# Kernel tuning notes

Measured on AMD Instinct MI355X. Metric: run time of the kernel, lower is better.

Reference implementation:

```python
import jax, jax.numpy as jnp
import numpy as np

N_NODES = 50000
N_EDGES = 800000
HDIM = 128
N_RELS = 24


def setup_inputs() -> dict:
    key = jax.random.key(0)
    ks = jax.random.split(key, 7)
    h = jax.random.normal(ks[0], (N_NODES, HDIM), dtype=jnp.float32)
    # per-relation weights ('simple' regularizer: independent matrix per relation)
    W = jax.random.normal(ks[1], (N_RELS, HDIM, HDIM), dtype=jnp.float32) / np.sqrt(HDIM)
    W_loop = jax.random.normal(ks[2], (HDIM, HDIM), dtype=jnp.float32) / np.sqrt(HDIM)
    bias = jax.random.normal(ks[3], (HDIM,), dtype=jnp.float32) * 0.02
    src = jax.random.randint(ks[4], (N_EDGES,), 0, N_NODES, dtype=jnp.int32)
    dst = jax.random.randint(ks[5], (N_EDGES,), 0, N_NODES, dtype=jnp.int32)
    rel = jax.random.randint(ks[6], (N_EDGES,), 0, N_RELS, dtype=jnp.int32)
    return {"h": h, "W": W, "W_loop": W_loop, "bias": bias,
            "src": src, "dst": dst, "rel": rel}


def reference(h, W, W_loop, bias, src, dst, rel):
    """RGCN.forward(g, step=0): one RelGraphConv layer.

    msg_e  = h[src_e] @ W[rel_e]          (per-relation transform)
    agg_v  = mean_{e: dst_e = v} msg_e    (mean aggregation)
    out_v  = relu(agg_v + h_v @ W_loop + bias)   (self-loop + activation)
    skip=False, dropout=0 -> no skip-average, dropout is identity.
    """
    N, D = h.shape
    # Transform all node features by every relation matrix once: (R, N, D).
    # Then each edge gathers its (relation, source) row -- avoids gathering
    # a per-edge (E, D, D) weight tensor.
    Hr = jnp.einsum('nd,rde->rne', h, W)          # (R, N, D)
    msg = Hr[rel, src]                            # (E, D) gathered messages
    agg = jax.ops.segment_sum(msg, dst, num_segments=N)            # (N, D)
    deg = jax.ops.segment_sum(jnp.ones((msg.shape[0],), h.dtype), dst,
                              num_segments=N)                      # (N,)
    agg = agg / jnp.maximum(deg, 1.0)[:, None]    # mean aggregation
    out = jax.nn.relu(agg + h @ W_loop + bias)
    return out
```

## Files before the change

### kernel.cpp

```cpp
#include <hip/hip_runtime.h>
#include <hip/hip_bf16.h>

#define N_NODES 50000
#define N_EDGES 800000
#define HDIM    128
#define N_RELS  24

#define MAX_TILES  12524
#define SORTED_CAP (MAX_TILES * 64)
#define NSCAN_BLK  196
#define TPB        4

typedef __attribute__((ext_vector_type(8))) short bf16x8;
typedef __attribute__((ext_vector_type(4))) float f32x4;
typedef __attribute__((ext_vector_type(4))) unsigned int u32x4;

static __device__ __forceinline__ float bfbits2f(unsigned u) {
    return __uint_as_float(u << 16);
}
static __device__ __forceinline__ unsigned f2bfbits(float x) {
    union { __hip_bfloat16 b; unsigned short u; } cv;
    cv.b = __float2bfloat16(x);
    return (unsigned)cv.u;
}



__global__ void k_setup(const float* __restrict__ h,
                        const float* __restrict__ W,
                        const float* __restrict__ Wl,
                        const int* __restrict__ rel,
                        const int* __restrict__ dst,
                        unsigned short* __restrict__ hb,
                        unsigned short* __restrict__ Wbt,
                        unsigned short* __restrict__ Wlbt,
                        int* __restrict__ degi,
                        int* __restrict__ meta)
{
    __shared__ int lh[N_RELS];
    if (threadIdx.x < N_RELS) lh[threadIdx.x] = 0;
    __syncthreads();

    int stride = gridDim.x * blockDim.x;
    int tid = blockIdx.x * blockDim.x + threadIdx.x;

    const float4* h4 = (const float4*)h;
    for (int i = tid; i < N_NODES * HDIM / 4; i += stride) {
        float4 v = h4[i];
        uint2 o;
        o.x = f2bfbits(v.x) | (f2bfbits(v.y) << 16);
        o.y = f2bfbits(v.z) | (f2bfbits(v.w) << 16);
        ((uint2*)hb)[i] = o;
    }
    for (int i = tid; i < N_RELS * HDIM * HDIM / 4; i += stride) {
        int r = i >> 12, rem = i & 4095;
        int e = rem >> 5, kq = rem & 31;
        const float* wp = W + (r << 14) + (kq << 9) + e;
        uint2 o;
        o.x = f2bfbits(wp[0])   | (f2bfbits(wp[128]) << 16);
        o.y = f2bfbits(wp[256]) | (f2bfbits(wp[384]) << 16);
        ((uint2*)Wbt)[i] = o;
    }
    for (int i = tid; i < HDIM * HDIM / 4; i += stride) {
        int e = i >> 5, kq = i & 31;
        const float* wp = Wl + (kq << 9) + e;
        uint2 o;
        o.x = f2bfbits(wp[0])   | (f2bfbits(wp[128]) << 16);
        o.y = f2bfbits(wp[256]) | (f2bfbits(wp[384]) << 16);
        ((uint2*)Wlbt)[i] = o;
    }
    for (int e = tid; e < N_EDGES; e += stride) {
        atomicAdd(&lh[rel[e]], 1);
        atomicAdd(&degi[dst[e]], 1);
    }
    __syncthreads();
    if (threadIdx.x < N_RELS) atomicAdd(&meta[threadIdx.x], lh[threadIdx.x]);
}


__global__ __launch_bounds__(256) void k_bsum(const int* __restrict__ degi,
                                              int* __restrict__ bsum)
{
    int i = blockIdx.x * 256 + threadIdx.x;
    int v = (i < N_NODES) ? degi[i] : 0;
    #pragma unroll
    for (int d = 32; d > 0; d >>= 1) v += __shfl_down(v, d);
    __shared__ int ws4[4];
    int lane = threadIdx.x & 63, wv = threadIdx.x >> 6;
    if (lane == 0) ws4[wv] = v;
    __syncthreads();
    if (threadIdx.x == 0)
        bsum[blockIdx.x] = ws4[0] + ws4[1] + ws4[2] + ws4[3];
}

__global__ __launch_bounds__(256) void k_scan_misc(int* __restrict__ meta,
                                                   const int* __restrict__ bsum,
                                                   int* __restrict__ boff,
                                                   int* __restrict__ seg)
{
    __shared__ int wsum[4];
    int t = threadIdx.x;
    int v = (t < NSCAN_BLK) ? bsum[t] : 0;
    int lane = t & 63, wv = t >> 6;
    int x = v;
    #pragma unroll
    for (int d = 1; d < 64; d <<= 1) {
        int y = __shfl_up(x, d);
        if (lane >= d) x += y;
    }
    if (lane == 63) wsum[wv] = x;
    __syncthreads();
    int add = 0;
    for (int w = 0; w < wv; ++w) add += wsum[w];
    if (t < NSCAN_BLK) boff[t] = add + x - v;
    if (t == NSCAN_BLK - 1) seg[N_NODES] = add + x;

    if (t == 0) {
        int run = 0;
        for (int r = 0; r < N_RELS; ++r) {
            int cnt = meta[r];
            meta[64 + r] = run;
            meta[96 + r] = run >> 6;
            run += ((cnt + 63) >> 6) << 6;
        }
        meta[64 + N_RELS] = run;
        meta[96 + N_RELS] = run >> 6;
    }
}

__global__ __launch_bounds__(256) void k_seg(const int* __restrict__ degi,
                                             const int* __restrict__ boff,
                                             int* __restrict__ seg,
                                             int* __restrict__ cursor)
{
    int i = blockIdx.x * 256 + threadIdx.x;
    int lane = threadIdx.x & 63, wv = threadIdx.x >> 6;
    int v = (i < N_NODES) ? degi[i] : 0;
    int x = v;
    #pragma unroll
    for (int d = 1; d < 64; d <<= 1) {
        int y = __shfl_up(x, d);
        if (lane >= d) x += y;
    }
    __shared__ int wpart[4];
    if (lane == 63) wpart[wv] = x;
    __syncthreads();
    int add = 0;
    for (int w = 0; w < wv; ++w) add += wpart[w];
    int s = boff[blockIdx.x] + add + x - v;
    if (i < N_NODES) { seg[i] = s; cursor[i] = s; }
}


__global__ void k_scatter(const int* __restrict__ rel,
                          const int* __restrict__ dst,
                          const int* __restrict__ src,
                          int* __restrict__ meta,
                          int* __restrict__ sorted,
                          int* __restrict__ cursor,
                          int2* __restrict__ edinfo)
{
    __shared__ int lh[N_RELS], lb[N_RELS];
    if (threadIdx.x < N_RELS) lh[threadIdx.x] = 0;
    __syncthreads();
    int e = blockIdx.x * blockDim.x + threadIdx.x;
    int r = 0, my = 0;
    bool valid = (e < N_EDGES);
    if (valid) {
        r = rel[e];
        my = atomicAdd(&lh[r], 1);
    }
    __syncthreads();
    if (threadIdx.x < N_RELS)
        lb[threadIdx.x] = atomicAdd(&meta[32 + threadIdx.x], lh[threadIdx.x]);
    __syncthreads();
    if (valid) {
        int pos = meta[64 + r] + lb[r] + my;
        sorted[pos] = e;
        int slot = atomicAdd(&cursor[dst[e]], 1);
        edinfo[pos] = make_int2(src[e], slot);
    }
}


__global__ __launch_bounds__(256) void k_edgeA(
    const unsigned short* __restrict__ hb,
    const unsigned short* __restrict__ Wbt,
    const int2* __restrict__ edinfo,
    const int* __restrict__ meta,
    unsigned int* __restrict__ msg)
{
    __shared__ __align__(16) unsigned char Ws[128 * 256];

    int ntiles = meta[96 + N_RELS];
    int b0 = blockIdx.x * TPB;
    if (b0 >= ntiles) return;

    int t = threadIdx.x;
    int lane = t & 63, wave = t >> 6;
    int l15 = lane & 15, l4 = lane >> 4;

    int rcur = -1;
    for (int bt = 0; bt < TPB; ++bt) {
        int b = b0 + bt;
        if (b >= ntiles) break;
        int r = rcur < 0 ? 0 : rcur;
        while (b >= meta[96 + r + 1]) ++r;
        int lbase = (b - meta[96 + r]) << 6;
        int lim = meta[r] - lbase;
        if (lim > 64) lim = 64;

        if (r != rcur) {
            if (bt > 0) __syncthreads();
            int row = t >> 1, half = t & 1;
            const uint4* g = (const uint4*)((const char*)Wbt + (size_t)r * 32768 + row * 256);
            unsigned sw = (row & 7) << 4;
            #pragma unroll
            for (int j = 0; j < 8; ++j) {
                int cb = (half << 7) + (j << 4);
                *(uint4*)(Ws + row * 256 + (cb ^ sw)) = g[cb >> 4];
            }
            rcur = r;
            __syncthreads();
        }

        int arow = (wave << 4) + l15;
        int srow = 0;
        if (arow < lim) srow = edinfo[(b << 6) + arow].x;
        const char* ap = (const char*)hb + (size_t)srow * 256 + (l4 << 4);
        bf16x8 a0 = *(const bf16x8*)(ap);
        bf16x8 a1 = *(const bf16x8*)(ap + 64);
        bf16x8 a2 = *(const bf16x8*)(ap + 128);
        bf16x8 a3 = *(const bf16x8*)(ap + 192);

        f32x4 acc[8];
        #pragma unroll
        for (int c = 0; c < 8; ++c) acc[c] = (f32x4)0.0f;

        #pragma unroll
        for (int kk = 0; kk < 4; ++kk) {
            int kb = (kk << 6) + (l4 << 4);
            bf16x8 a = (kk == 0) ? a0 : (kk == 1) ? a1 : (kk == 2) ? a2 : a3;
            #pragma unroll
            for (int c = 0; c < 8; ++c) {
                int brow = (c << 4) + l15;
                bf16x8 bb = *(const bf16x8*)(Ws + brow * 256 + (kb ^ ((brow & 7) << 4)));
                acc[c] = __builtin_amdgcn_mfma_f32_16x16x32_bf16(a, bb, acc[c], 0, 0, 0);
            }
        }

        #pragma unroll
        for (int i = 0; i < 4; ++i) {
            int m = (wave << 4) + (l4 << 2) + i;
            if (m < lim) {
                int slot = edinfo[(b << 6) + m].y;
                u32x4 o;
                o.x = f2bfbits(acc[0][i]) | (f2bfbits(acc[1][i]) << 16);
                o.y = f2bfbits(acc[2][i]) | (f2bfbits(acc[3][i]) << 16);
                o.z = f2bfbits(acc[4][i]) | (f2bfbits(acc[5][i]) << 16);
                o.w = f2bfbits(acc[6][i]) | (f2bfbits(acc[7][i]) << 16);
                __builtin_nontemporal_store(o,
                    (u32x4*)((char*)msg + (size_t)slot * 256 + (l15 << 4)));
            }
        }
    }
}


__global__ __launch_bounds__(256) void k_agg(
    const unsigned int* __restrict__ msg,
    const int* __restrict__ seg,
    unsigned short* __restrict__ aggB)
{
    int wv = threadIdx.x >> 6, lane = threadIdx.x & 63;
    int n = blockIdx.x * 4 + wv;
    if (n >= N_NODES) return;
    int s0 = seg[n], s1 = seg[n + 1];
    int deg = s1 - s0;
    int l4 = lane >> 4, l15 = lane & 15;

    float acc[8] = {0, 0, 0, 0, 0, 0, 0, 0};
    const char* base = (const char*)msg + (size_t)s0 * 256;
    int nit = (deg + 3) >> 2;
    for (int it = 0; it < nit; ++it) {
        if (it * 4 + l4 < deg) {
            u32x4 v = __builtin_nontemporal_load(
                (const u32x4*)(base + (size_t)it * 1024 + lane * 16));
            acc[0] += bfbits2f(v.x & 0xffff); acc[1] += bfbits2f(v.x >> 16);
            acc[2] += bfbits2f(v.y & 0xffff); acc[3] += bfbits2f(v.y >> 16);
            acc[4] += bfbits2f(v.z & 0xffff); acc[5] += bfbits2f(v.z >> 16);
            acc[6] += bfbits2f(v.w & 0xffff); acc[7] += bfbits2f(v.w >> 16);
        }
    }
    #pragma unroll
    for (int k = 0; k < 8; ++k) {
        acc[k] += __shfl_xor(acc[k], 16);
        acc[k] += __shfl_xor(acc[k], 32);
    }
    if (l4 == 0) {
        float inv = 1.0f / fmaxf((float)deg, 1.0f);
        u32x4 u;
        u.x = f2bfbits(acc[0] * inv) | (f2bfbits(acc[1] * inv) << 16);
        u.y = f2bfbits(acc[2] * inv) | (f2bfbits(acc[3] * inv) << 16);
        u.z = f2bfbits(acc[4] * inv) | (f2bfbits(acc[5] * inv) << 16);
        u.w = f2bfbits(acc[6] * inv) | (f2bfbits(acc[7] * inv) << 16);
        *(u32x4*)((char*)aggB + (size_t)n * 256 + l15 * 16) = u;
    }
}


__global__ __launch_bounds__(256) void k_selfA(
    const unsigned short* __restrict__ hb,
    const unsigned short* __restrict__ Wlbt,
    const float* __restrict__ bias,
    const unsigned short* __restrict__ aggB,
    float* __restrict__ out)
{
    __shared__ __align__(16) unsigned char Ws[128 * 256];
    __shared__ float biasS[128];

    int b = blockIdx.x, t = threadIdx.x;
    int n0 = b << 6;
    int lane = t & 63, wave = t >> 6;
    int l15 = lane & 15, l4 = lane >> 4;

    if (t < 128) biasS[t] = bias[t];

    int arow = (wave << 4) + l15;
    int va = n0 + arow; if (va > N_NODES - 1) va = N_NODES - 1;
    const char* ap = (const char*)hb + (size_t)va * 256 + (l4 << 4);
    bf16x8 a0 = *(const bf16x8*)(ap);
    bf16x8 a1 = *(const bf16x8*)(ap + 64);
    bf16x8 a2 = *(const bf16x8*)(ap + 128);
    bf16x8 a3 = *(const bf16x8*)(ap + 192);

    {
        int row = t >> 1, half = t & 1;
        const uint4* g = (const uint4*)((const char*)Wlbt + row * 256);
        unsigned sw = (row & 7) << 4;
        #pragma unroll
        for (int j = 0; j < 8; ++j) {
            int cb = (half << 7) + (j << 4);
            *(uint4*)(Ws + row * 256 + (cb ^ sw)) = g[cb >> 4];
        }
    }
    __syncthreads();

    f32x4 acc[8];
    #pragma unroll
    for (int c = 0; c < 8; ++c) acc[c] = (f32x4)0.0f;

    #pragma unroll
    for (int kk = 0; kk < 4; ++kk) {
        int kb = (kk << 6) + (l4 << 4);
        bf16x8 a = (kk == 0) ? a0 : (kk == 1) ? a1 : (kk == 2) ? a2 : a3;
        #pragma unroll
        for (int c = 0; c < 8; ++c) {
            int brow = (c << 4) + l15;
            bf16x8 bb = *(const bf16x8*)(Ws + brow * 256 + (kb ^ ((brow & 7) << 4)));
            acc[c] = __builtin_amdgcn_mfma_f32_16x16x32_bf16(a, bb, acc[c], 0, 0, 0);
        }
    }

    #pragma unroll
    for (int c = 0; c < 8; ++c) {
        #pragma unroll
        for (int i = 0; i < 4; ++i) {
            int m = (wave << 4) + (l4 << 2) + i;
            int v = n0 + m;
            if (v < N_NODES) {
                int col = (c << 4) + l15;
                float ag = bfbits2f(aggB[(size_t)v * 128 + l15 * 8 + ((c >> 1) << 1) + (c & 1)]);
                float val = acc[c][i] + ag + biasS[col];
                out[(size_t)v * 128 + col] = fmaxf(val, 0.0f);
            }
        }
    }
}


__global__ __launch_bounds__(256) void k_edgeB(
    const unsigned short* __restrict__ hb,
    const unsigned short* __restrict__ Wbt,
    const int* __restrict__ src,
    const int* __restrict__ dst,
    const int* __restrict__ sorted,
    const int* __restrict__ meta,
    float* __restrict__ agg)
{
    __shared__ __align__(16) unsigned char Ws[128 * 256];

    int b = blockIdx.x;
    if (b >= meta[96 + N_RELS]) return;
    int r = 0;
    while (b >= meta[96 + r + 1]) ++r;
    int lbase = (b - meta[96 + r]) << 6;
    int lim = meta[r] - lbase;
    if (lim > 64) lim = 64;

    int t = threadIdx.x;
    int lane = t & 63, wave = t >> 6;
    int l15 = lane & 15, l4 = lane >> 4;

    int arow = (wave << 4) + l15;
    int srow = 0;
    if (arow < lim) srow = src[sorted[(b << 6) + arow]];
    const char* ap = (const char*)hb + (size_t)srow * 256 + (l4 << 4);
    bf16x8 a0 = *(const bf16x8*)(ap);
    bf16x8 a1 = *(const bf16x8*)(ap + 64);
    bf16x8 a2 = *(const bf16x8*)(ap + 128);
    bf16x8 a3 = *(const bf16x8*)(ap + 192);

    {
        int row = t >> 1, half = t & 1;
        const uint4* g = (const uint4*)((const char*)Wbt + (size_t)r * 32768 + row * 256);
        unsigned sw = (row & 7) << 4;
        #pragma unroll
        for (int j = 0; j < 8; ++j) {
            int cb = (half << 7) + (j << 4);
            *(uint4*)(Ws + row * 256 + (cb ^ sw)) = g[cb >> 4];
        }
    }
    __syncthreads();

    f32x4 acc[8];
    #pragma unroll
    for (int c = 0; c < 8; ++c) acc[c] = (f32x4)0.0f;

    #pragma unroll
    for (int kk = 0; kk < 4; ++kk) {
        int kb = (kk << 6) + (l4 << 4);
        bf16x8 a = (kk == 0) ? a0 : (kk == 1) ? a1 : (kk == 2) ? a2 : a3;
        #pragma unroll
        for (int c = 0; c < 8; ++c) {
            int brow = (c << 4) + l15;
            bf16x8 bb = *(const bf16x8*)(Ws + brow * 256 + (kb ^ ((brow & 7) << 4)));
            acc[c] = __builtin_amdgcn_mfma_f32_16x16x32_bf16(a, bb, acc[c], 0, 0, 0);
        }
    }

    #pragma unroll
    for (int i = 0; i < 4; ++i) {
        int m = (wave << 4) + (l4 << 2) + i;
        if (m < lim) {
            int d = dst[sorted[(b << 6) + m]];
            #pragma unroll
            for (int c = 0; c < 8; ++c)
                atomicAdd(&agg[(size_t)d * 128 + (c << 4) + l15], acc[c][i]);
        }
    }
}

__global__ __launch_bounds__(256) void k_selfB(
    const unsigned short* __restrict__ hb,
    const unsigned short* __restrict__ Wlbt,
    const float* __restrict__ bias,
    const int* __restrict__ degi,
    float* __restrict__ agg)
{
    __shared__ __align__(16) unsigned char Ws[128 * 256];
    __shared__ float biasS[128];

    int b = blockIdx.x, t = threadIdx.x;
    int n0 = b << 6;
    int lane = t & 63, wave = t >> 6;
    int l15 = lane & 15, l4 = lane >> 4;

    if (t < 128) biasS[t] = bias[t];

    int arow = (wave << 4) + l15;
    int va = n0 + arow; if (va > N_NODES - 1) va = N_NODES - 1;
    const char* ap = (const char*)hb + (size_t)va * 256 + (l4 << 4);
    bf16x8 a0 = *(const bf16x8*)(ap);
    bf16x8 a1 = *(const bf16x8*)(ap + 64);
    bf16x8 a2 = *(const bf16x8*)(ap + 128);
    bf16x8 a3 = *(const bf16x8*)(ap + 192);

    {
        int row = t >> 1, half = t & 1;
        const uint4* g = (const uint4*)((const char*)Wlbt + row * 256);
        unsigned sw = (row & 7) << 4;
        #pragma unroll
        for (int j = 0; j < 8; ++j) {
            int cb = (half << 7) + (j << 4);
            *(uint4*)(Ws + row * 256 + (cb ^ sw)) = g[cb >> 4];
        }
    }
    __syncthreads();

    f32x4 acc[8];
    #pragma unroll
    for (int c = 0; c < 8; ++c) acc[c] = (f32x4)0.0f;

    #pragma unroll
    for (int kk = 0; kk < 4; ++kk) {
        int kb = (kk << 6) + (l4 << 4);
        bf16x8 a = (kk == 0) ? a0 : (kk == 1) ? a1 : (kk == 2) ? a2 : a3;
        #pragma unroll
        for (int c = 0; c < 8; ++c) {
            int brow = (c << 4) + l15;
            bf16x8 bb = *(const bf16x8*)(Ws + brow * 256 + (kb ^ ((brow & 7) << 4)));
            acc[c] = __builtin_amdgcn_mfma_f32_16x16x32_bf16(a, bb, acc[c], 0, 0, 0);
        }
    }

    #pragma unroll
    for (int c = 0; c < 8; ++c) {
        #pragma unroll
        for (int i = 0; i < 4; ++i) {
            int m = (wave << 4) + (l4 << 2) + i;
            int v = n0 + m;
            if (v < N_NODES) {
                int col = (c << 4) + l15;
                float inv = 1.0f / fmaxf((float)degi[v], 1.0f);
                float val = acc[c][i] + agg[(size_t)v * 128 + col] * inv + biasS[col];
                agg[(size_t)v * 128 + col] = fmaxf(val, 0.0f);
            }
        }
    }
}


extern "C" void kernel_launch(void* const* d_in, const int* in_sizes, int n_in,
                              void* d_out, int out_size, void* d_ws, size_t ws_size,
                              hipStream_t stream)
{
    (void)in_sizes; (void)n_in; (void)out_size;

    const float* h    = (const float*)d_in[0];
    const float* W    = (const float*)d_in[1];
    const float* Wl   = (const float*)d_in[2];
    const float* bias = (const float*)d_in[3];
    const int*   src  = (const int*)d_in[4];
    const int*   dst  = (const int*)d_in[5];
    const int*   rel  = (const int*)d_in[6];
    float* out = (float*)d_out;

    char* ws = (char*)d_ws;
    size_t off = 0;
    auto take = [&](size_t bytes) -> char* {
        char* p = ws + off;
        off += (bytes + 255) & ~(size_t)255;
        return p;
    };
    unsigned short* hb   = (unsigned short*)take((size_t)N_NODES * HDIM * 2);
    unsigned short* Wbt  = (unsigned short*)take((size_t)N_RELS * HDIM * HDIM * 2);
    unsigned short* Wlbt = (unsigned short*)take((size_t)HDIM * HDIM * 2);
    int*   degi    = (int*)take((size_t)N_NODES * 4);
    int*   meta    = (int*)take(1024);
    int*   sorted  = (int*)take((size_t)SORTED_CAP * 4);
    int*   seg     = (int*)take((size_t)(N_NODES + 1) * 4);
    int*   cursor  = (int*)take((size_t)N_NODES * 4);
    int*   bsum    = (int*)take((size_t)NSCAN_BLK * 4);
    int*   boff    = (int*)take((size_t)NSCAN_BLK * 4);
    int2*  edinfo  = (int2*)take((size_t)SORTED_CAP * 8);
    unsigned int*   msg  = (unsigned int*)take((size_t)N_EDGES * HDIM * 2);
    unsigned short* aggB = (unsigned short*)take((size_t)N_NODES * HDIM * 2);
    size_t big_need = off;

    bool pathA = (ws_size >= big_need);

    size_t zbytes = (size_t)((char*)meta - (char*)degi) + 1024;
    (void)hipMemsetAsync(degi, 0, zbytes, stream);

    k_setup<<<2048, 256, 0, stream>>>(h, W, Wl, rel, dst, hb, Wbt, Wlbt, degi, meta);
    k_bsum<<<NSCAN_BLK, 256, 0, stream>>>(degi, bsum);
    k_scan_misc<<<1, 256, 0, stream>>>(meta, bsum, boff, seg);
    k_seg<<<NSCAN_BLK, 256, 0, stream>>>(degi, boff, seg, cursor);
    k_scatter<<<(N_EDGES + 255) / 256, 256, 0, stream>>>(rel, dst, src, meta, sorted, cursor, edinfo);

    if (pathA) {
        k_edgeA<<<(MAX_TILES + TPB - 1) / TPB, 256, 0, stream>>>(hb, Wbt, edinfo, meta, msg);
        k_agg<<<(N_NODES + 3) / 4, 256, 0, stream>>>(msg, seg, aggB);
        k_selfA<<<(N_NODES + 63) / 64, 256, 0, stream>>>(hb, Wlbt, bias, aggB, out);
    } else {
        (void)hipMemsetAsync(out, 0, (size_t)N_NODES * HDIM * 4, stream);
        k_edgeB<<<MAX_TILES, 256, 0, stream>>>(hb, Wbt, src, dst, sorted, meta, out);
        k_selfB<<<(N_NODES + 63) / 64, 256, 0, stream>>>(hb, Wlbt, bias, degi, out);
    }
}
```

Measured before the change: 334.4 us.

## Prefetch next tile's gathered rows in edgeA and skip unused sorted writes

The edge-transform kernel now software-pipelines its tile loop: the gathered source rows for the next 64-edge tile are loaded into registers while the current tile's MFMAs run. Relation lookup becomes a monotone pointer instead of a per-tile rescan. Tiles per block rise from 4 to 8, and the scatter kernel skips writing the sorted edge-index array when the fast path does not need it. The aim is to hide gather latency and cut redundant global writes, at the cost of more registers and fewer blocks for load balancing.

```diff
diff --git a/kernel.cpp b/kernel.cpp
--- a/kernel.cpp
+++ b/kernel.cpp
@@ -9,7 +9,7 @@
 #define MAX_TILES  12524
 #define SORTED_CAP (MAX_TILES * 64)
 #define NSCAN_BLK  196
-#define TPB        4
+#define TPB        8
 
 typedef __attribute__((ext_vector_type(8))) short bf16x8;
 typedef __attribute__((ext_vector_type(4))) float f32x4;
@@ -158,7 +158,8 @@
                           int* __restrict__ meta,
                           int* __restrict__ sorted,
                           int* __restrict__ cursor,
-                          int2* __restrict__ edinfo)
+                          int2* __restrict__ edinfo,
+                          int writeSorted)
 {
     __shared__ int lh[N_RELS], lb[N_RELS];
     if (threadIdx.x < N_RELS) lh[threadIdx.x] = 0;
@@ -176,7 +177,7 @@
     __syncthreads();
     if (valid) {
         int pos = meta[64 + r] + lb[r] + my;
-        sorted[pos] = e;
+        if (writeSorted) sorted[pos] = e;
         int slot = atomicAdd(&cursor[dst[e]], 1);
         edinfo[pos] = make_int2(src[e], slot);
     }
@@ -195,43 +196,63 @@
     int ntiles = meta[96 + N_RELS];
     int b0 = blockIdx.x * TPB;
     if (b0 >= ntiles) return;
+    int ntloc = ntiles - b0; if (ntloc > TPB) ntloc = TPB;
 
     int t = threadIdx.x;
     int lane = t & 63, wave = t >> 6;
     int l15 = lane & 15, l4 = lane >> 4;
+    int arow = (wave << 4) + l15;
+
+    int rptr = 0;
+    while (b0 >= meta[96 + rptr + 1]) ++rptr;
+
+    int rA = rptr;
+    int limA = meta[rA] - ((b0 - meta[96 + rA]) << 6);
+    if (limA > 64) limA = 64;
+    bf16x8 c0, c1, c2, c3;
+    {
+        int srow = (arow < limA) ? edinfo[(b0 << 6) + arow].x : 0;
+        const char* ap = (const char*)hb + (size_t)srow * 256 + (l4 << 4);
+        c0 = *(const bf16x8*)(ap);
+        c1 = *(const bf16x8*)(ap + 64);
+        c2 = *(const bf16x8*)(ap + 128);
+        c3 = *(const bf16x8*)(ap + 192);
+    }
 
     int rcur = -1;
-    for (int bt = 0; bt < TPB; ++bt) {
+    for (int bt = 0; bt < ntloc; ++bt) {
         int b = b0 + bt;
-        if (b >= ntiles) break;
-        int r = rcur < 0 ? 0 : rcur;
-        while (b >= meta[96 + r + 1]) ++r;
-        int lbase = (b - meta[96 + r]) << 6;
-        int lim = meta[r] - lbase;
-        if (lim > 64) lim = 64;
-
-        if (r != rcur) {
+        bool havnext = (bt + 1 < ntloc);
+
+        int rN = rA, limN = 0;
+        bf16x8 n0 = c0, n1 = c1, n2 = c2, n3 = c3;
+        if (havnext) {
+            int bn = b + 1;
+            while (bn >= meta[96 + rptr + 1]) ++rptr;
+            rN = rptr;
+            limN = meta[rN] - ((bn - meta[96 + rN]) << 6);
+            if (limN > 64) limN = 64;
+            int srow = (arow < limN) ? edinfo[(bn << 6) + arow].x : 0;
+            const char* ap = (const char*)hb + (size_t)srow * 256 + (l4 << 4);
+            n0 = *(const bf16x8*)(ap);
+            n1 = *(const bf16x8*)(ap + 64);
+            n2 = *(const bf16x8*)(ap + 128);
+            n3 = *(const bf16x8*)(ap + 192);
+        }
+
+        if (rA != rcur) {
             if (bt > 0) __syncthreads();
             int row = t >> 1, half = t & 1;
-            const uint4* g = (const uint4*)((const char*)Wbt + (size_t)r * 32768 + row * 256);
+            const uint4* g = (const uint4*)((const char*)Wbt + (size_t)rA * 32768 + row * 256);
             unsigned sw = (row & 7) << 4;
             #pragma unroll
             for (int j = 0; j < 8; ++j) {
                 int cb = (half << 7) + (j << 4);
                 *(uint4*)(Ws + row * 256 + (cb ^ sw)) = g[cb >> 4];
             }
-            rcur = r;
+            rcur = rA;
             __syncthreads();
         }
-
-        int arow = (wave << 4) + l15;
-        int srow = 0;
-        if (arow < lim) srow = edinfo[(b << 6) + arow].x;
-        const char* ap = (const char*)hb + (size_t)srow * 256 + (l4 << 4);
-        bf16x8 a0 = *(const bf16x8*)(ap);
-        bf16x8 a1 = *(const bf16x8*)(ap + 64);
-        bf16x8 a2 = *(const bf16x8*)(ap + 128);
-        bf16x8 a3 = *(const bf16x8*)(ap + 192);
 
         f32x4 acc[8];
         #pragma unroll
@@ -240,7 +261,7 @@
         #pragma unroll
         for (int kk = 0; kk < 4; ++kk) {
             int kb = (kk << 6) + (l4 << 4);
-            bf16x8 a = (kk == 0) ? a0 : (kk == 1) ? a1 : (kk == 2) ? a2 : a3;
+            bf16x8 a = (kk == 0) ? c0 : (kk == 1) ? c1 : (kk == 2) ? c2 : c3;
             #pragma unroll
             for (int c = 0; c < 8; ++c) {
                 int brow = (c << 4) + l15;
@@ -252,7 +273,7 @@
         #pragma unroll
         for (int i = 0; i < 4; ++i) {
             int m = (wave << 4) + (l4 << 2) + i;
-            if (m < lim) {
+            if (m < limA) {
                 int slot = edinfo[(b << 6) + m].y;
                 u32x4 o;
                 o.x = f2bfbits(acc[0][i]) | (f2bfbits(acc[1][i]) << 16);
@@ -263,6 +284,9 @@
                     (u32x4*)((char*)msg + (size_t)slot * 256 + (l15 << 4)));
             }
         }
+
+        c0 = n0; c1 = n1; c2 = n2; c3 = n3;
+        rA = rN; limA = limN;
     }
 }
 
@@ -567,7 +591,8 @@
     k_bsum<<<NSCAN_BLK, 256, 0, stream>>>(degi, bsum);
     k_scan_misc<<<1, 256, 0, stream>>>(meta, bsum, boff, seg);
     k_seg<<<NSCAN_BLK, 256, 0, stream>>>(degi, boff, seg, cursor);
-    k_scatter<<<(N_EDGES + 255) / 256, 256, 0, stream>>>(rel, dst, src, meta, sorted, cursor, edinfo);
+    k_scatter<<<(N_EDGES + 255) / 256, 256, 0, stream>>>(rel, dst, src, meta, sorted, cursor,
+                                                         edinfo, pathA ? 0 : 1);
 
     if (pathA) {
         k_edgeA<<<(MAX_TILES + TPB - 1) / TPB, 256, 0, stream>>>(hb, Wbt, edinfo, meta, msg);
```

New measurement: 336.4 us. About the same (+0.6%).
